# Kernel tuning notes

Hardware: AMD Instinct MI355X
Metric: run time of the kernel (lower is better)

Reference implementation:

```python
import jax, jax.numpy as jnp
import numpy as np

B = 128  # batch


def _genperm(key, n):
    k1, k2 = jax.random.split(key)
    perm = jax.random.permutation(k1, n).astype(jnp.int32)
    scale = jax.random.uniform(k2, (n,), jnp.float32, 0.5, 2.0)
    return perm, scale


def _enc(x, p, s):  # y = A x with A[i, p[i]] = s[i]  (generalized permutation)
    return s * x[..., p]


def _dec(y, p, s):  # x = A^{-1} y
    return (y / s)[..., jnp.argsort(p)]


def _kconv(y, pin, sin, pout, sout, w, b, chw, stride):
    C, H, W = chw
    x = _dec(y, pin, sin)[:, :-1].reshape(-1, C, H, W)  # drop homogeneous 1
    pad = (w.shape[-1] - 1) // 2
    out = jax.lax.conv_general_dilated(x, w, (stride, stride), [(pad, pad), (pad, pad)],
                                       dimension_numbers=('NCHW', 'OIHW', 'NCHW'))
    out = out + b[None, :, None, None]
    flat = out.reshape(out.shape[0], -1)
    flat = jnp.concatenate([flat, jnp.ones((flat.shape[0], 1), flat.dtype)], axis=1)
    return _enc(flat, pout, sout)


def _krelu(y, pa, sa, pb, sb):  # B * relu(A^{-1} y); relu(1)=1 preserves homogeneous elt
    return _enc(jax.nn.relu(_dec(y, pa, sa)), pb, sb)


def _klin(y, pin, sin, pout, sout, W, b):
    x = _dec(y, pin, sin)[:, :-1]
    out = x @ W.T + b
    out = jnp.concatenate([out, jnp.ones((out.shape[0], 1), out.dtype)], axis=1)
    return _enc(out, pout, sout)


def setup_inputs():
    key = jax.random.key(0)
    ks = iter(jax.random.split(key, 64))
    d = {}
    N = {'0': 3 * 32 * 32 + 1, '1': 96 * 32 * 32 + 1, '3': 96 * 16 * 16 + 1,
         '4': 192 * 16 * 16 + 1, '6': 192 * 8 * 8 + 1, '9': 10 * 8 * 8 + 1,
         '10': 101, '11': 11}
    for name, n in [('0', N['0']), ('1a', N['1']), ('1b', N['1']), ('3a', N['3']),
                    ('3b', N['3']), ('4a', N['4']), ('4b', N['4']), ('6a', N['6']),
                    ('6b', N['6']), ('9a', N['9']), ('9b', N['9']), ('10a', N['10']),
                    ('10b', N['10']), ('11', N['11'])]:
        p, s = _genperm(next(ks), n)
        d['p' + name] = p
        d['s' + name] = s
    convs = [('1', (96, 3, 3, 3)), ('2', (96, 96, 3, 3)), ('3', (96, 96, 3, 3)),
             ('4', (192, 96, 3, 3)), ('5', (192, 192, 3, 3)), ('6', (192, 192, 3, 3)),
             ('7', (192, 192, 3, 3)), ('8', (192, 192, 1, 1)), ('9', (10, 192, 1, 1))]
    for name, shp in convs:
        fan_in = float(np.prod(shp[1:]))
        d['w' + name] = jax.random.normal(next(ks), shp, jnp.float32) / np.sqrt(fan_in)
        d['b' + name] = 0.01 * jax.random.normal(next(ks), (shp[0],), jnp.float32)
    d['fw1'] = jax.random.normal(next(ks), (100, 640), jnp.float32) / np.sqrt(640.0)
    d['fb1'] = 0.01 * jax.random.normal(next(ks), (100,), jnp.float32)
    d['fw2'] = jax.random.normal(next(ks), (10, 100), jnp.float32) / np.sqrt(100.0)
    d['fb2'] = 0.01 * jax.random.normal(next(ks), (10,), jnp.float32)
    x0 = jax.random.normal(next(ks), (B, 3 * 32 * 32), jnp.float32)
    x0h = jnp.concatenate([x0, jnp.ones((B, 1), jnp.float32)], axis=1)
    d['A0x0_affine'] = _enc(x0h, d['p0'], d['s0'])
    return d


def reference(A0x0_affine, w1, b1, w2, b2, w3, b3, w4, b4, w5, b5, w6, b6, w7, b7,
              w8, b8, w9, b9, fw1, fb1, fw2, fb2,
              p0, s0, p1a, s1a, p1b, s1b, p3a, s3a, p3b, s3b, p4a, s4a, p4b, s4b,
              p6a, s6a, p6b, s6b, p9a, s9a, p9b, s9b, p10a, s10a, p10b, s10b, p11, s11):
    y = _kconv(A0x0_affine, p0, s0, p1a, s1a, w1, b1, (3, 32, 32), 1)
    y = _krelu(y, p1a, s1a, p1b, s1b)                     # relu1
    y = _kconv(y, p1b, s1b, p1a, s1a, w2, b2, (96, 32, 32), 1)
    y = _krelu(y, p1a, s1a, p1b, s1b)                     # relu1 (reused)
    y = _kconv(y, p1b, s1b, p3a, s3a, w3, b3, (96, 32, 32), 2)   # conv3 (bn fused)
    y = _krelu(y, p3a, s3a, p3b, s3b)                     # relu3
    y = _kconv(y, p3b, s3b, p4a, s4a, w4, b4, (96, 16, 16), 1)
    y = _krelu(y, p4a, s4a, p4b, s4b)                     # relu4
    y = _kconv(y, p4b, s4b, p4a, s4a, w5, b5, (192, 16, 16), 1)
    y = _krelu(y, p4a, s4a, p4b, s4b)                     # relu4 (reused)
    y = _kconv(y, p4b, s4b, p6a, s6a, w6, b6, (192, 16, 16), 2)  # conv6 (bn fused)
    y = _krelu(y, p6a, s6a, p6b, s6b)                     # relu6
    y = _kconv(y, p6b, s6b, p6a, s6a, w7, b7, (192, 8, 8), 1)
    y = _krelu(y, p6a, s6a, p6b, s6b)                     # relu6 (reused)
    y = _kconv(y, p6b, s6b, p6a, s6a, w8, b8, (192, 8, 8), 1)
    y = _krelu(y, p6a, s6a, p6b, s6b)                     # relu6 (reused)
    y = _kconv(y, p6b, s6b, p9a, s9a, w9, b9, (192, 8, 8), 1)
    y = _krelu(y, p9a, s9a, p9b, s9b)                     # relu9
    y = _klin(y, p9b, s9b, p10a, s10a, fw1, fb1)          # fc1
    y = _krelu(y, p10a, s10a, p10b, s10b)                 # relu10
    y = _klin(y, p10b, s10b, p11, s11, fw2, fb2)          # fc2
    return y  # keyed output, shape (B, 11)
```

## Files before the change

kernel.cpp:

```cpp
#include <hip/hip_runtime.h>
#include <hip/hip_bf16.h>

#define BATCH 128
#define CDIV(a, b) (((a) + (b) - 1) / (b))

typedef __attribute__((ext_vector_type(8))) short short8;
typedef __attribute__((ext_vector_type(4))) float f32x4;

template <int V> struct ic { static constexpr int value = V; };
template <int... I> struct iseq {};
template <int N, int... I> struct mkseq : mkseq<N - 1, N - 1, I...> {};
template <int... I> struct mkseq<0, I...> { using type = iseq<I...>; };
template <class F, int... I>
__device__ __forceinline__ void unroll_all(F&& f, iseq<I...>) { (f(ic<I>{}), ...); }

__device__ __forceinline__ void gload_lds16(const void* g, void* l) {
    __builtin_amdgcn_global_load_lds(
        (const __attribute__((address_space(1))) void*)g,
        (__attribute__((address_space(3))) void*)l, 16, 0, 0);
}

__global__ void fill0_f32(float* __restrict__ p, int n) {
    int i = blockIdx.x * blockDim.x + threadIdx.x;
    if (i < n) p[i] = 0.0f;
}

__global__ void decode_kernel(const float* __restrict__ y, const int* __restrict__ p,
                              const float* __restrict__ s, float* __restrict__ x) {
    const int n = 3073;
    int idx = blockIdx.x * blockDim.x + threadIdx.x;
    if (idx >= BATCH * n) return;
    int i = idx % n, b = idx / n;
    int pi = p[i];
    if (pi >= 3072) return;
    float v = y[(size_t)b * n + i] / s[i];
    int c = pi >> 10; int r = pi & 1023; int h = r >> 5; int w = r & 31;
    x[((size_t)(b * 34 + h + 1) * 34 + (w + 1)) * 4 + c] = v;
}

struct HaloDesc { __hip_bfloat16* p; int Hp, Wp, C; };
struct Halo4 { HaloDesc d[4]; int cum[5]; int n; };

__global__ void halo_zero_multi(Halo4 h) {
    int idx = blockIdx.x * 256 + threadIdx.x;
    if (idx >= h.cum[h.n]) return;
    int seg = 0;
    while (idx >= h.cum[seg + 1]) ++seg;
    int local = idx - h.cum[seg];
    HaloDesc d = h.d[seg];
    int perB = (2 * d.Wp + 2 * (d.Hp - 2)) * d.C / 8;
    int b = local / perB;
    int r = (local % perB) * 8;
    int WpC = d.Wp * d.C;
    long addr;
    if (r < WpC) {
        addr = (long)(b * d.Hp) * WpC + r;
    } else if (r < 2 * WpC) {
        addr = (long)(b * d.Hp + d.Hp - 1) * WpC + (r - WpC);
    } else {
        int r3 = r - 2 * WpC;
        int sideN = (d.Hp - 2) * d.C;
        int side = r3 / sideN;
        int r4 = r3 % sideN;
        int row = 1 + r4 / d.C, c = r4 % d.C;
        addr = ((long)(b * d.Hp + row) * d.Wp + (side ? d.Wp - 1 : 0)) * d.C + c;
    }
    *(uint4*)((char*)d.p + addr * 2) = uint4{0, 0, 0, 0};
}

struct WtSeg { const float* src; __hip_bfloat16* dst; int Cout, Cin, KK, CoutPad; };
struct Wt8 { WtSeg s[8]; int cum[9]; };

__global__ void wt_transform_multi(Wt8 w) {
    int idx = blockIdx.x * 256 + threadIdx.x;
    if (idx >= w.cum[8]) return;
    int seg = 0;
    while (idx >= w.cum[seg + 1]) ++seg;
    int local = idx - w.cum[seg];
    WtSeg sg = w.s[seg];
    int c2 = local % 32; int t = local / 32;
    int co = t % sg.CoutPad; int t2 = t / sg.CoutPad;
    int KS = sg.Cin / 32;
    int kk = t2 % KS; int pos = t2 / KS;
    int cin = kk * 32 + c2;
    float v = (co < sg.Cout) ? sg.src[((size_t)co * sg.Cin + cin) * sg.KK + pos] : 0.0f;
    sg.dst[local] = __float2bfloat16(v);
}

__global__ __launch_bounds__(256) void conv1_kernel(
    const float* __restrict__ in, const float* __restrict__ w,
    const float* __restrict__ bias, __hip_bfloat16* __restrict__ out) {
    __shared__ float ws[96 * 27];
    __shared__ float bs[96];
    for (int i = threadIdx.x; i < 96 * 27; i += 256) ws[i] = w[i];
    if (threadIdx.x < 96) bs[threadIdx.x] = bias[threadIdx.x];
    __syncthreads();
    int idx = blockIdx.x * 256 + threadIdx.x;
    int q = idx & 3; int pix = idx >> 2;
    int b = pix >> 10, r = pix & 1023, oh = r >> 5, ow = r & 31;
    const float* ib = in + ((size_t)(b * 34 + oh) * 34 + ow) * 4;
    float patch[9][3];
#pragma unroll
    for (int ph = 0; ph < 3; ++ph)
#pragma unroll
        for (int pw = 0; pw < 3; ++pw) {
            float4 v = *(const float4*)(ib + ((size_t)ph * 34 + pw) * 4);
            patch[ph * 3 + pw][0] = v.x; patch[ph * 3 + pw][1] = v.y; patch[ph * 3 + pw][2] = v.z;
        }
    const int c0 = q * 24;
    float acc[24];
#pragma unroll
    for (int j = 0; j < 24; ++j) acc[j] = bs[c0 + j];
    for (int j = 0; j < 24; ++j) {
        const float* wc = &ws[(c0 + j) * 27];
#pragma unroll
        for (int ci = 0; ci < 3; ++ci)
#pragma unroll
            for (int pos = 0; pos < 9; ++pos)
                acc[j] = fmaf(patch[pos][ci], wc[ci * 9 + pos], acc[j]);
    }
    __hip_bfloat16* ob = out + ((size_t)(b * 34 + oh + 1) * 34 + ow + 1) * 96 + c0;
#pragma unroll
    for (int g = 0; g < 3; ++g) {
        union { uint4 u; unsigned short s[8]; } pk;
#pragma unroll
        for (int e = 0; e < 8; ++e) {
            __hip_bfloat16 hv = __float2bfloat16(fmaxf(acc[g * 8 + e], 0.0f));
            pk.s[e] = *(unsigned short*)&hv;
        }
        *(uint4*)(ob + g * 8) = pk.u;
    }
}

template <int CIN, int COUT, int HIN, int WIN, int STRIDE, int R,
          int BMPIX, int WM, int WN, int THREADS, int MINW>
__global__ __launch_bounds__(THREADS, MINW) void conv_gemm(
    const __hip_bfloat16* __restrict__ in,
    const __hip_bfloat16* __restrict__ wt,
    const float* __restrict__ bias,
    __hip_bfloat16* __restrict__ out) {
    constexpr int HOUT = HIN / STRIDE, WOUT = WIN / STRIDE;
    constexpr int Hp = HIN + 2, Wp = WIN + 2;
    constexpr int Hpo = HOUT + 2, Wpo = WOUT + 2;
    constexpr int D = 2 * R + 1;
    constexpr int KS = CIN / 32;
    constexpr int NSTEP = D * D * KS;
    constexpr int WAVES = THREADS / 64;
    static_assert(WAVES == WM * WN, "wave grid");
    constexpr int MT = BMPIX / WM / 16;
    constexpr int NTW = COUT / WN / 16;
    constexpr int AU = BMPIX * 4;
    constexpr int BU = COUT * 4;
    constexpr int APW = AU / WAVES;
    static_assert(APW % 64 == 0, "A stage divides");
    constexpr int AG = APW / 64;
    constexpr int BPW = BU / WAVES;
    constexpr int BG = BPW / 64;
    constexpr int BREM = BPW % 64;

    __shared__ short8 ldsA[2 * AU];
    __shared__ short8 ldsB[2 * BU];

    int wid = threadIdx.x >> 6;
    int lane = threadIdx.x & 63;
    int col = lane & 15, kgrp = lane >> 4;
    int wm = wid / WN, wn = wid % WN;
    int n0 = wn * (NTW * 16);

    const __hip_bfloat16* aSrc[AG];
#pragma unroll
    for (int i = 0; i < AG; ++i) {
        int u = wid * APW + i * 64 + lane;
        int p = u >> 2, q = u & 3;
        int gp = blockIdx.x * BMPIX + p;
        int b = gp / (HOUT * WOUT);
        int r = gp % (HOUT * WOUT);
        int oh = r / WOUT, ow = r % WOUT;
        aSrc[i] = in + ((size_t)(b * Hp + oh * STRIDE + 1 - R) * Wp + ow * STRIDE + 1 - R) * CIN + q * 8;
    }
    int bOff[BG + 1];
#pragma unroll
    for (int i = 0; i < BG + (BREM ? 1 : 0); ++i) {
        int u = wid * BPW + i * 64 + lane;
        bOff[i] = (u >> 2) * 32 + (u & 3) * 8;
    }

    auto stage = [&](int aoff, size_t woff, int buf) {
#pragma unroll
        for (int i = 0; i < AG; ++i)
            gload_lds16(aSrc[i] + aoff, &ldsA[buf * AU + wid * APW + i * 64]);
#pragma unroll
        for (int i = 0; i < BG; ++i)
            gload_lds16(wt + woff + bOff[i], &ldsB[buf * BU + wid * BPW + i * 64]);
        if constexpr (BREM > 0) {
            if (lane < BREM)
                gload_lds16(wt + woff + bOff[BG], &ldsB[buf * BU + wid * BPW + BG * 64]);
        }
    };
    auto stepA = [](int s) {
        int pos = s / KS, kk = s - (s / KS) * KS;
        return ((pos / D) * Wp + (pos % D)) * CIN + kk * 32;
    };

    f32x4 acc[MT][NTW] = {};

    stage(stepA(0), 0, 0);
    __syncthreads();

    unroll_all([&](auto sc) {
        constexpr int s = decltype(sc)::value;
        if constexpr (s + 1 < NSTEP)
            stage(stepA(s + 1), (size_t)(s + 1) * (COUT * 32), (s + 1) & 1);
        constexpr int buf = s & 1;
        short8 af[MT], bf[NTW];
#pragma unroll
        for (int mt = 0; mt < MT; ++mt)
            af[mt] = ldsA[buf * AU + (wm * MT * 16 + mt * 16 + col) * 4 + kgrp];
#pragma unroll
        for (int nt = 0; nt < NTW; ++nt)
            bf[nt] = ldsB[buf * BU + (n0 + nt * 16 + col) * 4 + kgrp];
#pragma unroll
        for (int nt = 0; nt < NTW; ++nt)
#pragma unroll
            for (int mt = 0; mt < MT; ++mt)
                acc[mt][nt] = __builtin_amdgcn_mfma_f32_16x16x32_bf16(
                    af[mt], bf[nt], acc[mt][nt], 0, 0, 0);
        __syncthreads();
    }, typename mkseq<NSTEP>::type{});

#pragma unroll
    for (int mt = 0; mt < MT; ++mt) {
#pragma unroll
        for (int nt = 0; nt < NTW; ++nt) {
            int cout = n0 + nt * 16 + col;
            float bv = bias[cout];
#pragma unroll
            for (int rg = 0; rg < 4; ++rg) {
                int p = wm * MT * 16 + mt * 16 + kgrp * 4 + rg;
                int gp = blockIdx.x * BMPIX + p;
                int b = gp / (HOUT * WOUT);
                int r = gp % (HOUT * WOUT);
                int oh = r / WOUT, ow = r % WOUT;
                float v = fmaxf(acc[mt][nt][rg] + bv, 0.0f);
                out[((size_t)(b * Hpo + oh + 1) * Wpo + ow + 1) * COUT + cout] =
                    __float2bfloat16(v);
            }
        }
    }
}

template <int CIN, int COUT, int HIN, int WIN, int STRIDE, int R,
          int WN, int MT, int NTW, int LA, int DEPTH, int THREADS, int MINW>
__global__ __launch_bounds__(THREADS, MINW) void conv_pipe(
    const __hip_bfloat16* __restrict__ in,
    const __hip_bfloat16* __restrict__ wt,
    const float* __restrict__ bias,
    __hip_bfloat16* __restrict__ out) {
    constexpr int HOUT = HIN / STRIDE, WOUT = WIN / STRIDE;
    constexpr int Hp = HIN + 2, Wp = WIN + 2;
    constexpr int Hpo = HOUT + 2, Wpo = WOUT + 2;
    constexpr int D = 2 * R + 1;
    constexpr int KS = CIN / 32;
    constexpr int NSTEP = D * D * KS;
    constexpr int WAVES = THREADS / 64;
    static_assert(WAVES == WN, "one wave row");
    constexpr int BM = MT * 16;
    constexpr int BN = WN * NTW * 16;
    static_assert(BN == COUT, "block covers full N");
    static_assert(BM % WOUT == 0, "whole output rows");
    constexpr int BMR = BM / WOUT;
    constexpr int SUPR = (BMR - 1) * STRIDE + D;
    constexpr int CINU = CIN / 8;
    constexpr int UPP = CINU + 1;
    constexpr int ROWU = Wp * CINU;
    constexpr int TOTU = SUPR * ROWU;

    __shared__ short8 ldsA[SUPR * Wp * UPP];
    __shared__ short8 ldsB[WAVES * DEPTH * NTW * 64];

    int wid = threadIdx.x >> 6;
    int lane = threadIdx.x & 63;
    int col = lane & 15, kgrp = lane >> 4;
    int n0 = wid * (NTW * 16);
    int su = col * 4 + kgrp;

    auto issueChunk = [&](int c, int slot) {
        const __hip_bfloat16* src = wt + ((size_t)c * COUT + n0) * 32 + lane * 8;
#pragma unroll
        for (int nt = 0; nt < NTW; ++nt)
            gload_lds16(src + nt * (16 * 32),
                        &ldsB[((wid * DEPTH + slot) * NTW + nt) * 64]);
    };

#pragma unroll
    for (int c = 0; c < LA; ++c)
        if (c < NSTEP) issueChunk(c, c % DEPTH);

    int m0 = blockIdx.x * BM;
    int gor = m0 / WOUT;
    int b = gor / HOUT;
    int oh0 = gor % HOUT;
    int r0 = oh0 * STRIDE + (1 - R);
    const __hip_bfloat16* gsrc = in + ((size_t)(b * Hp + r0) * Wp) * CIN;
    for (int g = threadIdx.x; g < TOTU; g += THREADS) {
        int row = g / ROWU;
        int ur = g - row * ROWU;
        int pix = ur / CINU;
        int c = ur - pix * CINU;
        ldsA[(row * Wp + pix) * UPP + c] = *reinterpret_cast<const short8*>(gsrc + (size_t)g * 8);
    }
    __syncthreads();

    int abaseu[MT];
#pragma unroll
    for (int mt = 0; mt < MT; ++mt) {
        int mloc = mt * 16 + col;
        int orow = mloc / WOUT, ocol = mloc % WOUT;
        abaseu[mt] = ((orow * STRIDE) * Wp + ocol * STRIDE + (1 - R)) * UPP + kgrp;
    }

    short8 af[3][MT], bf[3][NTW];
    f32x4 acc[MT][NTW] = {};

    auto readFrags = [&](int s, auto rIC) {
        constexpr int r = decltype(rIC)::value;
        int pos = s / KS, kk = s - (s / KS) * KS;
        int poff = ((pos / D) * Wp + (pos % D)) * UPP;
#pragma unroll
        for (int mt = 0; mt < MT; ++mt)
            af[r][mt] = ldsA[abaseu[mt] + poff + kk * 4];
        int slot = s % DEPTH;
#pragma unroll
        for (int nt = 0; nt < NTW; ++nt)
            bf[r][nt] = ldsB[((wid * DEPTH + slot) * NTW + nt) * 64 + su];
    };

    readFrags(0, ic<0>{});
    if (1 < NSTEP) readFrags(1, ic<1>{});

    unroll_all([&](auto sc) {
        constexpr int s = decltype(sc)::value;
        if constexpr (s + LA < NSTEP) issueChunk(s + LA, (s + LA) % DEPTH);
        if constexpr (s + 2 < NSTEP) {
            constexpr int I = (s + LA < NSTEP - 1) ? (s + LA) : (NSTEP - 1);
            constexpr int NW0 = (I - (s + 2)) * NTW;
            constexpr int NW = NW0 < 0 ? 0 : NW0;
            asm volatile("s_waitcnt vmcnt(%0)" :: "i"(NW) : "memory");
            readFrags(s + 2, ic<(s + 2) % 3>{});
        }
#pragma unroll
        for (int nt = 0; nt < NTW; ++nt)
#pragma unroll
            for (int mt = 0; mt < MT; ++mt)
                acc[mt][nt] = __builtin_amdgcn_mfma_f32_16x16x32_bf16(
                    af[s % 3][mt], bf[s % 3][nt], acc[mt][nt], 0, 0, 0);
    }, typename mkseq<NSTEP>::type{});

#pragma unroll
    for (int mt = 0; mt < MT; ++mt) {
#pragma unroll
        for (int nt = 0; nt < NTW; ++nt) {
            int cout = n0 + nt * 16 + col;
            float bv = bias[cout];
#pragma unroll
            for (int rg = 0; rg < 4; ++rg) {
                int mloc = mt * 16 + kgrp * 4 + rg;
                int orow = mloc / WOUT, ocol = mloc % WOUT;
                float v = fmaxf(acc[mt][nt][rg] + bv, 0.0f);
                out[((size_t)(b * Hpo + oh0 + orow + 1) * Wpo + ocol + 1) * COUT + cout] =
                    __float2bfloat16(v);
            }
        }
    }
}

template <int CIN, int COUT, int HIN, int WIN, int STRIDE, int R,
          int WM, int WN, int MT, int NTW, int PW, int THREADS, int MINW>
__global__ __launch_bounds__(THREADS, MINW) void conv_lds(
    const __hip_bfloat16* __restrict__ in,
    const __hip_bfloat16* __restrict__ wt,
    const float* __restrict__ bias,
    __hip_bfloat16* __restrict__ out) {
    constexpr int HOUT = HIN / STRIDE, WOUT = WIN / STRIDE;
    constexpr int Hp = HIN + 2, Wp = WIN + 2;
    constexpr int Hpo = HOUT + 2, Wpo = WOUT + 2;
    constexpr int D = 2 * R + 1;
    constexpr int KS = CIN / 32;
    constexpr int NSTEP = D * D * KS;
    constexpr int BM = WM * MT * 16;
    constexpr int BN = WN * NTW * 16;
    static_assert(BN == COUT, "block covers full N");
    static_assert(BM % WOUT == 0, "block tile = whole output rows");
    static_assert(THREADS / 64 == WM * WN, "wave count");
    constexpr int BMR = BM / WOUT;
    constexpr int SUPR = (BMR - 1) * STRIDE + D;
    constexpr int CINU = CIN / 8;
    constexpr int UPP = CINU + 1;
    constexpr int ROWU = Wp * CINU;
    constexpr int TOTU = SUPR * ROWU;

    __shared__ short8 lds[SUPR * Wp * UPP];

    int m0 = blockIdx.x * BM;
    int gor = m0 / WOUT;
    int b = gor / HOUT;
    int oh0 = gor % HOUT;
    int r0 = oh0 * STRIDE + (1 - R);

    const __hip_bfloat16* gsrc = in + ((size_t)(b * Hp + r0) * Wp) * CIN;
    for (int g = threadIdx.x; g < TOTU; g += THREADS) {
        int row = g / ROWU;
        int ur = g - row * ROWU;
        int pix = ur / CINU;
        int c = ur - pix * CINU;
        lds[(row * Wp + pix) * UPP + c] = *reinterpret_cast<const short8*>(gsrc + (size_t)g * 8);
    }
    __syncthreads();

    int wid = threadIdx.x >> 6;
    int lane = threadIdx.x & 63;
    int col = lane & 15, kgrp = lane >> 4;
    int wm = wid / WN, wn = wid % WN;
    int n0 = wn * NTW * 16;

    int apix[MT];
#pragma unroll
    for (int mt = 0; mt < MT; ++mt) {
        int mloc = (wm * MT + mt) * 16 + col;
        int orow = mloc / WOUT, ocol = mloc % WOUT;
        apix[mt] = (orow * STRIDE) * Wp + ocol * STRIDE + (1 - R);
    }
    const __hip_bfloat16* bbase[NTW];
#pragma unroll
    for (int nt = 0; nt < NTW; ++nt)
        bbase[nt] = wt + (size_t)(n0 + nt * 16 + col) * 32 + kgrp * 8;

    short8 abuf[3][MT];
    short8 bbuf[PW][NTW];
    f32x4 acc[MT][NTW] = {};

    auto ldA = [&](int s, int slot) {
        int pos = s / KS, kk = s - (s / KS) * KS;
        int dh = pos / D, dw = pos - dh * D;
        int poff = dh * Wp + dw;
#pragma unroll
        for (int mt = 0; mt < MT; ++mt)
            abuf[slot][mt] = lds[(apix[mt] + poff) * UPP + kk * 4 + kgrp];
    };
    auto ldB = [&](int s, int slot) {
        size_t off = (size_t)s * (COUT * 32);
#pragma unroll
        for (int nt = 0; nt < NTW; ++nt)
            bbuf[slot][nt] = *reinterpret_cast<const short8*>(bbase[nt] + off);
    };

#pragma unroll
    for (int s = 0; s < PW - 1; ++s)
        if (s < NSTEP) ldB(s, s);
    ldA(0, 0);
    if (1 < NSTEP) ldA(1, 1);
    __builtin_amdgcn_sched_barrier(0);

#pragma unroll
    for (int s = 0; s < NSTEP; ++s) {
        if (s + PW - 1 < NSTEP) ldB(s + PW - 1, (s + PW - 1) % PW);
        if (s + 2 < NSTEP) ldA(s + 2, (s + 2) % 3);
        __builtin_amdgcn_sched_barrier(0);
#pragma unroll
        for (int nt = 0; nt < NTW; ++nt)
#pragma unroll
            for (int mt = 0; mt < MT; ++mt)
                acc[mt][nt] = __builtin_amdgcn_mfma_f32_16x16x32_bf16(
                    abuf[s % 3][mt], bbuf[s % PW][nt], acc[mt][nt], 0, 0, 0);
    }

#pragma unroll
    for (int mt = 0; mt < MT; ++mt) {
#pragma unroll
        for (int nt = 0; nt < NTW; ++nt) {
            int cout = n0 + nt * 16 + col;
            float bv = bias[cout];
#pragma unroll
            for (int rg = 0; rg < 4; ++rg) {
                int mloc = (wm * MT + mt) * 16 + kgrp * 4 + rg;
                int orow = mloc / WOUT, ocol = mloc % WOUT;
                float v = fmaxf(acc[mt][nt][rg] + bv, 0.0f);
                out[((size_t)(b * Hpo + oh0 + orow + 1) * Wpo + ocol + 1) * COUT + cout] =
                    __float2bfloat16(v);
            }
        }
    }
}

__global__ __launch_bounds__(256) void conv9_kernel(
    const __hip_bfloat16* __restrict__ in, const __hip_bfloat16* __restrict__ wt,
    const float* __restrict__ bias, float* __restrict__ out) {
    int wid = threadIdx.x >> 6;
    int lane = threadIdx.x & 63;
    int wave = blockIdx.x * 4 + wid;
    int m0 = wave * 16;
    int col = lane & 15;
    int kgrp = lane >> 4;
    int m = m0 + col;
    int b = m >> 6; int r = m & 63; int oh = r >> 3; int ow = r & 7;
    const __hip_bfloat16* abase = in + ((size_t)(b * 10 + oh + 1) * 10 + ow + 1) * 192 + kgrp * 8;
    f32x4 acc = {};
#pragma unroll
    for (int kk = 0; kk < 6; ++kk) {
        short8 bfr = *reinterpret_cast<const short8*>(wt + ((size_t)kk * 16 + col) * 32 + kgrp * 8);
        short8 a = *reinterpret_cast<const short8*>(abase + kk * 32);
        acc = __builtin_amdgcn_mfma_f32_16x16x32_bf16(a, bfr, acc, 0, 0, 0);
    }
    if (col < 10) {
        float bv = bias[col];
#pragma unroll
        for (int rg = 0; rg < 4; ++rg) {
            int m2 = m0 + kgrp * 4 + rg;
            int b2 = m2 >> 6; int r2 = m2 & 63;
            out[(size_t)b2 * 640 + col * 64 + r2] = fmaxf(acc[rg] + bv, 0.0f);
        }
    }
}

__global__ __launch_bounds__(128) void head_kernel(
    const float* __restrict__ act9, const float* __restrict__ fw1, const float* __restrict__ fb1,
    const float* __restrict__ fw2, const float* __restrict__ fb2,
    const int* __restrict__ p11, const float* __restrict__ s11, float* __restrict__ out) {
    __shared__ float x[640];
    __shared__ float h[100];
    __shared__ float o[10];
    int b = blockIdx.x, t = threadIdx.x;
    for (int i = t; i < 160; i += 128)
        ((float4*)x)[i] = ((const float4*)(act9 + (size_t)b * 640))[i];
    __syncthreads();
    if (t < 100) {
        float acc = fb1[t];
        const float4* wr = (const float4*)(fw1 + (size_t)t * 640);
        const float4* xv = (const float4*)x;
#pragma unroll 4
        for (int i = 0; i < 160; ++i) {
            float4 wv = wr[i], qv = xv[i];
            acc = fmaf(wv.x, qv.x, acc); acc = fmaf(wv.y, qv.y, acc);
            acc = fmaf(wv.z, qv.z, acc); acc = fmaf(wv.w, qv.w, acc);
        }
        h[t] = fmaxf(acc, 0.0f);
    }
    __syncthreads();
    if (t < 10) {
        float acc = fb2[t];
        for (int i = 0; i < 100; ++i) acc = fmaf(h[i], fw2[t * 100 + i], acc);
        o[t] = acc;
    }
    __syncthreads();
    if (t < 11) {
        int pi = p11[t];
        out[(size_t)b * 11 + t] = s11[t] * (pi == 10 ? 1.0f : o[pi]);
    }
}

extern "C" void kernel_launch(void* const* d_in, const int* in_sizes, int n_in,
                              void* d_out, int out_size, void* d_ws, size_t ws_size,
                              hipStream_t stream) {
    const int*   p0  = (const int*)  d_in[0];
    const float* s0  = (const float*)d_in[1];
    const int*   p11 = (const int*)  d_in[26];
    const float* s11 = (const float*)d_in[27];
    const float* w1 = (const float*)d_in[28]; const float* b1 = (const float*)d_in[29];
    const float* w2 = (const float*)d_in[30]; const float* b2 = (const float*)d_in[31];
    const float* w3 = (const float*)d_in[32]; const float* b3 = (const float*)d_in[33];
    const float* w4 = (const float*)d_in[34]; const float* b4 = (const float*)d_in[35];
    const float* w5 = (const float*)d_in[36]; const float* b5 = (const float*)d_in[37];
    const float* w6 = (const float*)d_in[38]; const float* b6 = (const float*)d_in[39];
    const float* w7 = (const float*)d_in[40]; const float* b7 = (const float*)d_in[41];
    const float* w8 = (const float*)d_in[42]; const float* b8 = (const float*)d_in[43];
    const float* w9 = (const float*)d_in[44]; const float* b9 = (const float*)d_in[45];
    const float* fw1 = (const float*)d_in[46]; const float* fb1 = (const float*)d_in[47];
    const float* fw2 = (const float*)d_in[48]; const float* fb2 = (const float*)d_in[49];
    const float* A0 = (const float*)d_in[50];
    float* out = (float*)d_out;

    size_t off = 0;
    auto alloc = [&](size_t bytes) {
        void* p = (char*)d_ws + off;
        off += (bytes + 255) & ~(size_t)255;
        return p;
    };
    const size_t SZ_3434_96  = (size_t)BATCH * 34 * 34 * 96 * 2;
    const size_t SZ_1818_96  = (size_t)BATCH * 18 * 18 * 96 * 2;
    const size_t SZ_1818_192 = (size_t)BATCH * 18 * 18 * 192 * 2;

    float* dec = (float*)alloc((size_t)BATCH * 34 * 34 * 4 * 4);
    __hip_bfloat16* regA = (__hip_bfloat16*)alloc(SZ_3434_96);
    __hip_bfloat16* regB = (__hip_bfloat16*)alloc(SZ_3434_96);
    __hip_bfloat16* regC = (__hip_bfloat16*)alloc(SZ_1818_96);
    __hip_bfloat16* regD = (__hip_bfloat16*)alloc(SZ_1818_192);
    __hip_bfloat16* wt2 = (__hip_bfloat16*)alloc((size_t)9 * 96 * 96 * 2);
    __hip_bfloat16* wt3 = (__hip_bfloat16*)alloc((size_t)9 * 96 * 96 * 2);
    __hip_bfloat16* wt4 = (__hip_bfloat16*)alloc((size_t)9 * 192 * 96 * 2);
    __hip_bfloat16* wt5 = (__hip_bfloat16*)alloc((size_t)9 * 192 * 192 * 2);
    __hip_bfloat16* wt6 = (__hip_bfloat16*)alloc((size_t)9 * 192 * 192 * 2);
    __hip_bfloat16* wt7 = (__hip_bfloat16*)alloc((size_t)9 * 192 * 192 * 2);
    __hip_bfloat16* wt8 = (__hip_bfloat16*)alloc((size_t)1 * 192 * 192 * 2);
    __hip_bfloat16* wt9 = (__hip_bfloat16*)alloc((size_t)16 * 192 * 2);
    float* act9 = (float*)alloc((size_t)BATCH * 640 * 4);

    const int TPB = 256;

    int decN = BATCH * 34 * 34 * 4;
    fill0_f32<<<CDIV(decN, TPB), TPB, 0, stream>>>(dec, decN);
    decode_kernel<<<CDIV(BATCH * 3073, TPB), TPB, 0, stream>>>(A0, p0, s0, dec);

    Wt8 wts;
    wts.s[0] = {w2, wt2, 96, 96, 9, 96};
    wts.s[1] = {w3, wt3, 96, 96, 9, 96};
    wts.s[2] = {w4, wt4, 192, 96, 9, 192};
    wts.s[3] = {w5, wt5, 192, 192, 9, 192};
    wts.s[4] = {w6, wt6, 192, 192, 9, 192};
    wts.s[5] = {w7, wt7, 192, 192, 9, 192};
    wts.s[6] = {w8, wt8, 192, 192, 1, 192};
    wts.s[7] = {w9, wt9, 10, 192, 1, 16};
    wts.cum[0] = 0;
    for (int i = 0; i < 8; ++i)
        wts.cum[i + 1] = wts.cum[i] + wts.s[i].KK * wts.s[i].CoutPad * wts.s[i].Cin;
    wt_transform_multi<<<CDIV(wts.cum[8], TPB), TPB, 0, stream>>>(wts);

    auto chunks = [](int Hp, int Wp, int C) { return BATCH * (2 * Wp + 2 * (Hp - 2)) * C / 8; };
    Halo4 h0;
    h0.d[0] = {regA, 34, 34, 96};
    h0.d[1] = {regB, 34, 34, 96};
    h0.d[2] = {regC, 18, 18, 96};
    h0.d[3] = {regD, 18, 18, 192};
    h0.n = 4; h0.cum[0] = 0;
    for (int i = 0; i < 4; ++i)
        h0.cum[i + 1] = h0.cum[i] + chunks(h0.d[i].Hp, h0.d[i].Wp, h0.d[i].C);
    halo_zero_multi<<<CDIV(h0.cum[4], TPB), TPB, 0, stream>>>(h0);

    conv1_kernel<<<2048, 256, 0, stream>>>(dec, w1, b1, regA);
    conv_gemm<96, 96, 32, 32, 1, 1, 128, 2, 2, 256, 3><<<1024, 256, 0, stream>>>(regA, wt2, b2, regB);
    Halo4 h5; h5.d[0] = {regA, 18, 18, 192}; h5.n = 1;
    h5.cum[0] = 0; h5.cum[1] = chunks(18, 18, 192);
    halo_zero_multi<<<CDIV(h5.cum[1], TPB), TPB, 0, stream>>>(h5);
    conv_gemm<96, 96, 32, 32, 2, 1, 64, 2, 2, 256, 3><<<512, 256, 0, stream>>>(regB, wt3, b3, regC);
    conv_gemm<96, 192, 16, 16, 1, 1, 64, 1, 4, 256, 3><<<512, 256, 0, stream>>>(regC, wt4, b4, regD);
    Halo4 h6; h6.d[0] = {regC, 10, 10, 192}; h6.n = 1;
    h6.cum[0] = 0; h6.cum[1] = chunks(10, 10, 192);
    halo_zero_multi<<<CDIV(h6.cum[1], TPB), TPB, 0, stream>>>(h6);
    conv_gemm<192, 192, 16, 16, 1, 1, 64, 1, 4, 256, 3><<<512, 256, 0, stream>>>(regD, wt5, b5, regA);
    conv_pipe<192, 192, 16, 16, 2, 1, 4, 1, 3, 3, 3, 256, 2><<<512, 256, 0, stream>>>(regA, wt6, b6, regC);
    conv_pipe<192, 192, 8, 8, 1, 1, 4, 2, 3, 4, 4, 256, 2><<<256, 256, 0, stream>>>(regC, wt7, b7, regD);
    conv_lds<192, 192, 8, 8, 1, 0, 1, 4, 1, 3, 6, 256, 3><<<512, 256, 0, stream>>>(regD, wt8, b8, regB);
    conv9_kernel<<<128, 256, 0, stream>>>(regB, wt9, b9, act9);
    head_kernel<<<BATCH, 128, 0, stream>>>(act9, fw1, fb1, fw2, fb2, p11, s11, out);
}
```

Measured before the change: 218.8 us.

## Replace conv_gemm with 4-deep pipelined, XOR-swizzled unified LDS conv kernel

Replaces the double-buffered conv_gemm with conv_2ph. The new kernel uses a 4-slot LDS ring with lookahead 2, and A and B tiles share one staging buffer so every wave issues the same number of async global-to-LDS loads. Waiting is done with explicit vmcnt counts and a single barrier per step, in place of a full __syncthreads after the MFMAs. An XOR swizzle on LDS unit indices is meant to cut bank conflicts on fragment reads. Waves now split only along N, and conv2/conv3 move to 128-thread blocks with 64-pixel tiles, which changes occupancy and LDS use per block.

```diff
diff --git a/kernel.cpp b/kernel.cpp
--- a/kernel.cpp
+++ b/kernel.cpp
@@ -18,6 +18,14 @@
     __builtin_amdgcn_global_load_lds(
         (const __attribute__((address_space(1))) void*)g,
         (__attribute__((address_space(3))) void*)l, 16, 0, 0);
+}
+
+__device__ __forceinline__ int sig_u(int u) { return u ^ ((u >> 2) & 7); }
+__device__ __forceinline__ int inv_sig_u(int x) {
+    int r0 = ((x >> 2) ^ (x >> 4)) & 1;
+    int r1 = (x >> 3) & 1;
+    int r2 = (x >> 4) & 1;
+    return x ^ (r0 | (r1 << 1) | (r2 << 2));
 }
 
 __global__ void fill0_f32(float* __restrict__ p, int n) {
@@ -133,8 +141,8 @@
 }
 
 template <int CIN, int COUT, int HIN, int WIN, int STRIDE, int R,
-          int BMPIX, int WM, int WN, int THREADS, int MINW>
-__global__ __launch_bounds__(THREADS, MINW) void conv_gemm(
+          int BMPIX, int WN, int THREADS, int MINW>
+__global__ __launch_bounds__(THREADS, MINW) void conv_2ph(
     const __hip_bfloat16* __restrict__ in,
     const __hip_bfloat16* __restrict__ wt,
     const float* __restrict__ bias,
@@ -146,86 +154,93 @@
     constexpr int KS = CIN / 32;
     constexpr int NSTEP = D * D * KS;
     constexpr int WAVES = THREADS / 64;
-    static_assert(WAVES == WM * WN, "wave grid");
-    constexpr int MT = BMPIX / WM / 16;
-    constexpr int NTW = COUT / WN / 16;
-    constexpr int AU = BMPIX * 4;
-    constexpr int BU = COUT * 4;
-    constexpr int APW = AU / WAVES;
-    static_assert(APW % 64 == 0, "A stage divides");
-    constexpr int AG = APW / 64;
-    constexpr int BPW = BU / WAVES;
-    constexpr int BG = BPW / 64;
-    constexpr int BREM = BPW % 64;
-
-    __shared__ short8 ldsA[2 * AU];
-    __shared__ short8 ldsB[2 * BU];
+    static_assert(WAVES == WN, "wave count");
+    constexpr int MT = BMPIX / 16;
+    constexpr int NTW = COUT / (WN * 16);
+    constexpr int AUN = BMPIX * 4;
+    constexpr int BUN = COUT * 4;
+    constexpr int CUN = AUN + BUN;
+    constexpr int DEPTH = 4, LA = 2;
+    constexpr int LPW = CUN / (64 * WAVES);
+    static_assert(CUN % (64 * WAVES) == 0, "stage divides");
+    static_assert(AUN % 64 == 0, "A/B instr boundary aligned");
+
+    __shared__ short8 lds[DEPTH * CUN];
 
     int wid = threadIdx.x >> 6;
     int lane = threadIdx.x & 63;
     int col = lane & 15, kgrp = lane >> 4;
-    int wm = wid / WN, wn = wid % WN;
-    int n0 = wn * (NTW * 16);
-
-    const __hip_bfloat16* aSrc[AG];
-#pragma unroll
-    for (int i = 0; i < AG; ++i) {
-        int u = wid * APW + i * 64 + lane;
-        int p = u >> 2, q = u & 3;
-        int gp = blockIdx.x * BMPIX + p;
-        int b = gp / (HOUT * WOUT);
-        int r = gp % (HOUT * WOUT);
-        int oh = r / WOUT, ow = r % WOUT;
-        aSrc[i] = in + ((size_t)(b * Hp + oh * STRIDE + 1 - R) * Wp + ow * STRIDE + 1 - R) * CIN + q * 8;
-    }
-    int bOff[BG + 1];
-#pragma unroll
-    for (int i = 0; i < BG + (BREM ? 1 : 0); ++i) {
-        int u = wid * BPW + i * 64 + lane;
-        bOff[i] = (u >> 2) * 32 + (u & 3) * 8;
-    }
-
-    auto stage = [&](int aoff, size_t woff, int buf) {
-#pragma unroll
-        for (int i = 0; i < AG; ++i)
-            gload_lds16(aSrc[i] + aoff, &ldsA[buf * AU + wid * APW + i * 64]);
-#pragma unroll
-        for (int i = 0; i < BG; ++i)
-            gload_lds16(wt + woff + bOff[i], &ldsB[buf * BU + wid * BPW + i * 64]);
-        if constexpr (BREM > 0) {
-            if (lane < BREM)
-                gload_lds16(wt + woff + bOff[BG], &ldsB[buf * BU + wid * BPW + BG * 64]);
-        }
-    };
-    auto stepA = [](int s) {
+    int n0 = wid * (NTW * 16);
+
+    const __hip_bfloat16* aSrc[LPW];
+    int bOff[LPW];
+    bool isA[LPW];
+#pragma unroll
+    for (int i = 0; i < LPW; ++i) {
+        int x = (wid * LPW + i) * 64 + lane;
+        if (x < AUN) {
+            isA[i] = true;
+            int v = inv_sig_u(x);
+            int p = v >> 2, q = v & 3;
+            int gp = blockIdx.x * BMPIX + p;
+            int b = gp / (HOUT * WOUT);
+            int r = gp % (HOUT * WOUT);
+            int oh = r / WOUT, ow = r % WOUT;
+            aSrc[i] = in + ((size_t)(b * Hp + oh * STRIDE + 1 - R) * Wp
+                            + ow * STRIDE + 1 - R) * CIN + q * 8;
+            bOff[i] = 0;
+        } else {
+            isA[i] = false;
+            bOff[i] = inv_sig_u(x - AUN) * 8;
+            aSrc[i] = in;
+        }
+    }
+    int aRd[MT], bRd[NTW];
+#pragma unroll
+    for (int mt = 0; mt < MT; ++mt)
+        aRd[mt] = sig_u((mt * 16 + col) * 4 + kgrp);
+#pragma unroll
+    for (int nt = 0; nt < NTW; ++nt)
+        bRd[nt] = AUN + sig_u((n0 + nt * 16 + col) * 4 + kgrp);
+
+    auto stepAoff = [](int s) {
         int pos = s / KS, kk = s - (s / KS) * KS;
         return ((pos / D) * Wp + (pos % D)) * CIN + kk * 32;
     };
+    auto stage = [&](int s) {
+        int slot = s % DEPTH;
+        int aoff = stepAoff(s);
+        const __hip_bfloat16* wchunk = wt + (size_t)s * (COUT * 32);
+#pragma unroll
+        for (int i = 0; i < LPW; ++i) {
+            const __hip_bfloat16* src = isA[i] ? (aSrc[i] + aoff) : (wchunk + bOff[i]);
+            gload_lds16(src, &lds[slot * CUN + (wid * LPW + i) * 64]);
+        }
+    };
 
     f32x4 acc[MT][NTW] = {};
-
-    stage(stepA(0), 0, 0);
-    __syncthreads();
+    stage(0);
+    if constexpr (1 < NSTEP) stage(1);
 
     unroll_all([&](auto sc) {
         constexpr int s = decltype(sc)::value;
-        if constexpr (s + 1 < NSTEP)
-            stage(stepA(s + 1), (size_t)(s + 1) * (COUT * 32), (s + 1) & 1);
-        constexpr int buf = s & 1;
-        short8 af[MT], bf[NTW];
-#pragma unroll
-        for (int mt = 0; mt < MT; ++mt)
-            af[mt] = ldsA[buf * AU + (wm * MT * 16 + mt * 16 + col) * 4 + kgrp];
-#pragma unroll
-        for (int nt = 0; nt < NTW; ++nt)
-            bf[nt] = ldsB[buf * BU + (n0 + nt * 16 + col) * 4 + kgrp];
+        if constexpr (s + LA < NSTEP) stage(s + LA);
+        constexpr int C = (s + 1 < NSTEP ? 1 : 0) + (s + 2 < NSTEP ? 1 : 0);
+        asm volatile("s_waitcnt vmcnt(%0)" :: "i"(C * LPW) : "memory");
+        __builtin_amdgcn_s_barrier();
+        __builtin_amdgcn_sched_barrier(0);
+        constexpr int slot = s % DEPTH;
+        short8 af[MT], bfr[NTW];
+#pragma unroll
+        for (int mt = 0; mt < MT; ++mt) af[mt] = lds[slot * CUN + aRd[mt]];
+#pragma unroll
+        for (int nt = 0; nt < NTW; ++nt) bfr[nt] = lds[slot * CUN + bRd[nt]];
 #pragma unroll
         for (int nt = 0; nt < NTW; ++nt)
 #pragma unroll
             for (int mt = 0; mt < MT; ++mt)
                 acc[mt][nt] = __builtin_amdgcn_mfma_f32_16x16x32_bf16(
-                    af[mt], bf[nt], acc[mt][nt], 0, 0, 0);
-        __syncthreads();
+                    af[mt], bfr[nt], acc[mt][nt], 0, 0, 0);
     }, typename mkseq<NSTEP>::type{});
 
 #pragma unroll
@@ -236,7 +251,7 @@
             float bv = bias[cout];
 #pragma unroll
             for (int rg = 0; rg < 4; ++rg) {
-                int p = wm * MT * 16 + mt * 16 + kgrp * 4 + rg;
+                int p = mt * 16 + kgrp * 4 + rg;
                 int gp = blockIdx.x * BMPIX + p;
                 int b = gp / (HOUT * WOUT);
                 int r = gp % (HOUT * WOUT);
@@ -636,16 +651,16 @@
     halo_zero_multi<<<CDIV(h0.cum[4], TPB), TPB, 0, stream>>>(h0);
 
     conv1_kernel<<<2048, 256, 0, stream>>>(dec, w1, b1, regA);
-    conv_gemm<96, 96, 32, 32, 1, 1, 128, 2, 2, 256, 3><<<1024, 256, 0, stream>>>(regA, wt2, b2, regB);
+    conv_2ph<96, 96, 32, 32, 1, 1, 64, 2, 128, 2><<<2048, 128, 0, stream>>>(regA, wt2, b2, regB);
     Halo4 h5; h5.d[0] = {regA, 18, 18, 192}; h5.n = 1;
     h5.cum[0] = 0; h5.cum[1] = chunks(18, 18, 192);
     halo_zero_multi<<<CDIV(h5.cum[1], TPB), TPB, 0, stream>>>(h5);
-    conv_gemm<96, 96, 32, 32, 2, 1, 64, 2, 2, 256, 3><<<512, 256, 0, stream>>>(regB, wt3, b3, regC);
-    conv_gemm<96, 192, 16, 16, 1, 1, 64, 1, 4, 256, 3><<<512, 256, 0, stream>>>(regC, wt4, b4, regD);
+    conv_2ph<96, 96, 32, 32, 2, 1, 64, 2, 128, 2><<<512, 128, 0, stream>>>(regB, wt3, b3, regC);
+    conv_2ph<96, 192, 16, 16, 1, 1, 64, 4, 256, 2><<<512, 256, 0, stream>>>(regC, wt4, b4, regD);
     Halo4 h6; h6.d[0] = {regC, 10, 10, 192}; h6.n = 1;
     h6.cum[0] = 0; h6.cum[1] = chunks(10, 10, 192);
     halo_zero_multi<<<CDIV(h6.cum[1], TPB), TPB, 0, stream>>>(h6);
-    conv_gemm<192, 192, 16, 16, 1, 1, 64, 1, 4, 256, 3><<<512, 256, 0, stream>>>(regD, wt5, b5, regA);
+    conv_2ph<192, 192, 16, 16, 1, 1, 64, 4, 256, 2><<<512, 256, 0, stream>>>(regD, wt5, b5, regA);
     conv_pipe<192, 192, 16, 16, 2, 1, 4, 1, 3, 3, 3, 256, 2><<<512, 256, 0, stream>>>(regA, wt6, b6, regC);
     conv_pipe<192, 192, 8, 8, 1, 1, 4, 2, 3, 4, 4, 256, 2><<<256, 256, 0, stream>>>(regC, wt7, b7, regD);
     conv_lds<192, 192, 8, 8, 1, 0, 1, 4, 1, 3, 6, 256, 3><<<512, 256, 0, stream>>>(regD, wt8, b8, regB);
```

Result: faster. 200.1 us (-8.5%).
